# Optimization experiments

Measured on AMD Instinct MI355X. Metric: run time of the kernel, lower is better.

Reference implementation:

```python
import jax, jax.numpy as jnp
import numpy as np

INPUT_DIM = 512
HIDDEN_DIM = 1024
OUTPUT_DIM = 1000
BATCH = 256
SEQ_LEN = 256


def setup_inputs() -> dict:
    key = jax.random.key(0)
    ks = jax.random.split(key, 7)
    std = 1.0 / np.sqrt(HIDDEN_DIM)
    u = lambda k, shape: jax.random.uniform(k, shape, jnp.float32, -std, std)
    return {
        "x": jax.random.normal(ks[0], (BATCH, SEQ_LEN, INPUT_DIM), jnp.float32),
        "w_x2h": u(ks[1], (4 * HIDDEN_DIM, INPUT_DIM)),
        "b_x2h": u(ks[2], (4 * HIDDEN_DIM,)),
        "w_h2h": u(ks[3], (4 * HIDDEN_DIM, HIDDEN_DIM)),
        "b_h2h": u(ks[4], (4 * HIDDEN_DIM,)),
        "w_fc": u(ks[5], (OUTPUT_DIM, HIDDEN_DIM)),
        "b_fc": u(ks[6], (OUTPUT_DIM,)),
    }


def _lstm_last_hidden(x, w_x2h, b_x2h, w_h2h, b_h2h):
    B, T, D = x.shape
    H = w_h2h.shape[1]
    # Precompute input-to-hidden for all timesteps in one big GEMM: [B,T,4H]
    xg = jnp.einsum("btd,gd->btg", x, w_x2h) + b_x2h + b_h2h
    xg = jnp.swapaxes(xg, 0, 1)  # [T,B,4H] for scan

    def step(carry, xg_t):
        h, c = carry
        gates = xg_t + h @ w_h2h.T  # [B,4H]
        i, f, g, o = jnp.split(gates, 4, axis=1)
        i = jax.nn.sigmoid(i)
        f = jax.nn.sigmoid(f)
        g = jnp.tanh(g)
        o = jax.nn.sigmoid(o)
        c = c * f + i * g
        h = o * jnp.tanh(c)
        return (h, c), None

    h0 = jnp.zeros((B, H), x.dtype)
    c0 = jnp.zeros((B, H), x.dtype)
    (h_last, _), _ = jax.lax.scan(step, (h0, c0), xg)
    return h_last


def reference(x, w_x2h, b_x2h, w_h2h, b_h2h, w_fc, b_fc):
    h_last = _lstm_last_hidden(x, w_x2h, b_x2h, w_h2h, b_h2h)  # [B,H]
    return h_last @ w_fc.T + b_fc  # [B,OUTPUT_DIM]
```

## Files before the change

### kernel.cpp

```cpp
#include <hip/hip_runtime.h>

typedef __attribute__((ext_vector_type(8))) short short8;
typedef __attribute__((ext_vector_type(4))) float floatx4;

#define DIN  512
#define HSZ  1024
#define G4   4096
#define KTOT 1536
#define BQ   256
#define TT   256

#define MFMA __builtin_amdgcn_mfma_f32_16x16x32_bf16

__device__ __forceinline__ unsigned short f2bf(float f){
  unsigned int u = __float_as_uint(f);
  u += 0x7fffu + ((u >> 16) & 1u);
  return (unsigned short)(u >> 16);
}
__device__ __forceinline__ unsigned int pack2(float a, float b){
  return (unsigned int)f2bf(a) | ((unsigned int)f2bf(b) << 16);
}

__global__ void prep_wcat(const float* __restrict__ wx, const float* __restrict__ wh,
                          const float* __restrict__ bx, const float* __restrict__ bh,
                          unsigned short* __restrict__ Wcat, float* __restrict__ bias){
  int gid = blockIdx.x * blockDim.x + threadIdx.x;
  int idx = gid * 8;
  int g = idx / KTOT;
  int k = idx - g * KTOT;
  const float* src = (k < DIN) ? (wx + (size_t)g * DIN + k)
                               : (wh + (size_t)g * HSZ + (k - DIN));
  float4 f0 = *(const float4*)(src);
  float4 f1 = *(const float4*)(src + 4);
  uint4 v = make_uint4(pack2(f0.x,f0.y), pack2(f0.z,f0.w), pack2(f1.x,f1.y), pack2(f1.z,f1.w));
  *(uint4*)(Wcat + (size_t)g * KTOT + k) = v;
  if (gid < G4) bias[gid] = bx[gid] + bh[gid];
}

__global__ void prep_wfc(const float* __restrict__ wfc, unsigned short* __restrict__ Wfcb){
  int gid = blockIdx.x * blockDim.x + threadIdx.x;
  int idx = gid * 8;
  int n = idx >> 10;
  int k = idx & 1023;
  uint4 v;
  if (n < 1000){
    const float* src = wfc + (size_t)n * 1024 + k;
    float4 f0 = *(const float4*)(src);
    float4 f1 = *(const float4*)(src + 4);
    v = make_uint4(pack2(f0.x,f0.y), pack2(f0.z,f0.w), pack2(f1.x,f1.y), pack2(f1.z,f1.w));
  } else {
    v = make_uint4(0u, 0u, 0u, 0u);
  }
  *(uint4*)(Wfcb + idx) = v;
}

__global__ void prep_x(const float* __restrict__ x, unsigned short* __restrict__ xbf){
  int gid = blockIdx.x * 256 + threadIdx.x;
  int d8 = gid & 63;
  int b  = (gid >> 6) & 255;
  int t  = gid >> 14;
  const float* src = x + (((size_t)b * TT) + t) * DIN + d8 * 8;
  float4 f0 = *(const float4*)(src);
  float4 f1 = *(const float4*)(src + 4);
  uint4 v = make_uint4(pack2(f0.x,f0.y), pack2(f0.z,f0.w), pack2(f1.x,f1.y), pack2(f1.z,f1.w));
  *(uint4*)(xbf + (((size_t)t * BQ) + b) * DIN + d8 * 8) = v;
}

__global__ void init_misc(unsigned int* __restrict__ h0w, unsigned int* __restrict__ cnt, int ncnt){
  int gid = blockIdx.x * 256 + threadIdx.x;
  if (gid < 131072) h0w[gid] = 0u;
  if (gid < ncnt)   cnt[gid] = 0u;
}

__global__ __launch_bounds__(512, 2)
void lstm_persist(const unsigned short* __restrict__ xbf,
                  const unsigned short* __restrict__ Wcat,
                  const float* __restrict__ bias,
                  unsigned short* __restrict__ hseq,
                  unsigned int* __restrict__ cnt){
  extern __shared__ char smem[];
  char*  Ws  = smem;
  float* Gt2 = (float*)(smem + 98304);
  float* Bls = (float*)(smem + 98304 + 34816);

  const int tid  = threadIdx.x;
  const int bx   = blockIdx.x;
  const int bg   = bx >> 7;
  const int b0   = bg << 7;
  const int hb   = bx & 127;
  const int u0   = hb << 3;
  const int lane = tid & 63;
  const int w    = tid >> 6;
  const int kg   = w & 1;
  const int rg   = w >> 1;

  {
    int c  = tid >> 4;
    int ch = tid & 15;
    int grow = (c >> 3) * HSZ + u0 + (c & 7);
    const char* src = (const char*)(Wcat + (size_t)grow * KTOT);
    char* dst = Ws + c * 3072;
    int xr = (c & 7) << 4;
    #pragma unroll
    for (int q = 0; q < 12; ++q){
      int k2 = ch * 192 + q * 16;
      *(uint4*)(dst + (k2 ^ xr)) = *(const uint4*)(src + k2);
    }
    if (tid < 32) Bls[tid] = bias[(size_t)(tid >> 3) * HSZ + u0 + (tid & 7)];
  }
  __syncthreads();

  const int kq8  = (lane >> 4) * 8;
  const int cA   = lane & 15;
  const int cB   = 16 + (lane & 15);
  const char* bpA = Ws + cA * 3072; const int xorA = (cA & 7) << 4;
  const char* bpB = Ws + cB * 3072; const int xorB = (cB & 7) << 4;

  const size_t rowA0 = (size_t)(b0 + rg * 32 + (lane & 15));

  const int erow = tid >> 2;
  const int eup  = (tid & 3) * 2;
  float cst0 = 0.f, cst1 = 0.f;

  for (int t = 0; t < TT; ++t){
    const unsigned short* hin  = hseq + (size_t)t * (BQ * HSZ);
    unsigned short*       hout = hseq + (size_t)(t + 1) * (BQ * HSZ);

    floatx4 acc[2][2][2];
    #pragma unroll
    for (int ab = 0; ab < 2; ++ab)
      #pragma unroll
      for (int rf = 0; rf < 2; ++rf)
        #pragma unroll
        for (int cf = 0; cf < 2; ++cf)
          acc[ab][rf][cf] = (floatx4){0.f,0.f,0.f,0.f};

    short8 X0[8], X1[8];
    {
      const unsigned short* xr0p = xbf + ((size_t)t * BQ + rowA0) * DIN + kg * 256 + kq8;
      const unsigned short* xr1p = xr0p + 16 * DIN;
      #pragma unroll
      for (int p = 0; p < 8; ++p){
        X0[p] = *(const short8*)(xr0p + p * 32);
        X1[p] = *(const short8*)(xr1p + p * 32);
      }
    }
    __builtin_amdgcn_sched_barrier(0);

    if (t > 0){
      if (tid < 64){
        const unsigned int* cp = &cnt[(((size_t)t * 2 + bg) * 8) * 16];
        const int g16 = (lane & 7) * 16;
        while (true){
          unsigned int v = __hip_atomic_load(cp + g16, __ATOMIC_RELAXED, __HIP_MEMORY_SCOPE_AGENT);
          if (__ballot(v >= 16u) == ~0ull) break;
          __builtin_amdgcn_s_sleep(2);
        }
      }
      __syncthreads();
      asm volatile("" ::: "memory");
    }

    {
      const int bbase = kg * 512 + kq8 * 2;
      short8 bA[2], bB[2];
      bA[0] = *(const short8*)(bpA + ((bbase     ) ^ xorA));
      bB[0] = *(const short8*)(bpB + ((bbase     ) ^ xorB));
      bA[1] = *(const short8*)(bpA + ((bbase + 64) ^ xorA));
      bB[1] = *(const short8*)(bpB + ((bbase + 64) ^ xorB));
      #pragma unroll
      for (int j = 0; j < 8; ++j){
        const int sl = j & 1;
        short8 b0 = bA[sl], b1 = bB[sl];
        if (j < 6){
          int bb = bbase + (j + 2) * 64;
          bA[sl] = *(const short8*)(bpA + (bb ^ xorA));
          bB[sl] = *(const short8*)(bpB + (bb ^ xorB));
        }
        acc[sl][0][0] = MFMA(X0[j], b0, acc[sl][0][0], 0, 0, 0);
        acc[sl][0][1] = MFMA(X0[j], b1, acc[sl][0][1], 0, 0, 0);
        acc[sl][1][0] = MFMA(X1[j], b0, acc[sl][1][0], 0, 0, 0);
        acc[sl][1][1] = MFMA(X1[j], b1, acc[sl][1][1], 0, 0, 0);
      }
    }

    {
      const unsigned short* hr0 = hin + rowA0 * HSZ + kg * 512 + kq8;
      const unsigned short* hr1 = hr0 + (size_t)16 * HSZ;
      short8 A0[16], A1[16];
      #pragma unroll
      for (int p = 0; p < 16; ++p){
        A0[p] = *(const short8*)(hr0 + p * 32);
        A1[p] = *(const short8*)(hr1 + p * 32);
      }
      __builtin_amdgcn_sched_barrier(0);
      const int bbase = 1024 + kg * 1024 + kq8 * 2;
      short8 bA[2], bB[2];
      bA[0] = *(const short8*)(bpA + ((bbase     ) ^ xorA));
      bB[0] = *(const short8*)(bpB + ((bbase     ) ^ xorB));
      bA[1] = *(const short8*)(bpA + ((bbase + 64) ^ xorA));
      bB[1] = *(const short8*)(bpB + ((bbase + 64) ^ xorB));
      #pragma unroll
      for (int j = 0; j < 16; ++j){
        const int sl = j & 1;
        short8 b0 = bA[sl], b1 = bB[sl];
        if (j < 14){
          int bb = bbase + (j + 2) * 64;
          bA[sl] = *(const short8*)(bpA + (bb ^ xorA));
          bB[sl] = *(const short8*)(bpB + (bb ^ xorB));
        }
        acc[sl][0][0] = MFMA(A0[j], b0, acc[sl][0][0], 0, 0, 0);
        acc[sl][0][1] = MFMA(A0[j], b1, acc[sl][0][1], 0, 0, 0);
        acc[sl][1][0] = MFMA(A1[j], b0, acc[sl][1][0], 0, 0, 0);
        acc[sl][1][1] = MFMA(A1[j], b1, acc[sl][1][1], 0, 0, 0);
      }
    }

    {
      float* gdst = Gt2 + kg * (128 * 34);
      int r0 = rg * 32 + (lane >> 4) * 4;
      #pragma unroll
      for (int rf = 0; rf < 2; ++rf){
        floatx4 g0 = acc[0][rf][0] + acc[1][rf][0];
        floatx4 g1 = acc[0][rf][1] + acc[1][rf][1];
        #pragma unroll
        for (int r = 0; r < 4; ++r){
          gdst[(r0 + rf * 16 + r) * 34 + cA] = g0[r];
          gdst[(r0 + rf * 16 + r) * 34 + cB] = g1[r];
        }
      }
    }
    __syncthreads();

    {
      const float* g0p = Gt2 + erow * 34;
      const float* g1p = g0p + 128 * 34;
      float gi0 = g0p[     eup] + g1p[     eup] + Bls[     eup];
      float gf0 = g0p[ 8 + eup] + g1p[ 8 + eup] + Bls[ 8 + eup];
      float gg0 = g0p[16 + eup] + g1p[16 + eup] + Bls[16 + eup];
      float go0 = g0p[24 + eup] + g1p[24 + eup] + Bls[24 + eup];
      float gi1 = g0p[     eup + 1] + g1p[     eup + 1] + Bls[     eup + 1];
      float gf1 = g0p[ 8 + eup + 1] + g1p[ 8 + eup + 1] + Bls[ 8 + eup + 1];
      float gg1 = g0p[16 + eup + 1] + g1p[16 + eup + 1] + Bls[16 + eup + 1];
      float go1 = g0p[24 + eup + 1] + g1p[24 + eup + 1] + Bls[24 + eup + 1];

      float iv0 = 1.f / (1.f + __expf(-gi0));
      float fv0 = 1.f / (1.f + __expf(-gf0));
      float e20 = __expf(-2.f * fmaxf(fminf(gg0, 30.f), -30.f));
      float gv0 = (1.f - e20) / (1.f + e20);
      float ov0 = 1.f / (1.f + __expf(-go0));
      float cn0 = cst0 * fv0 + iv0 * gv0;
      cst0 = cn0;
      float ec0 = __expf(-2.f * fmaxf(fminf(cn0, 30.f), -30.f));
      float hv0 = ov0 * (1.f - ec0) / (1.f + ec0);

      float iv1 = 1.f / (1.f + __expf(-gi1));
      float fv1 = 1.f / (1.f + __expf(-gf1));
      float e21 = __expf(-2.f * fmaxf(fminf(gg1, 30.f), -30.f));
      float gv1 = (1.f - e21) / (1.f + e21);
      float ov1 = 1.f / (1.f + __expf(-go1));
      float cn1 = cst1 * fv1 + iv1 * gv1;
      cst1 = cn1;
      float ec1 = __expf(-2.f * fmaxf(fminf(cn1, 30.f), -30.f));
      float hv1 = ov1 * (1.f - ec1) / (1.f + ec1);

      __hip_atomic_store((unsigned int*)(hout + (size_t)(b0 + erow) * HSZ + u0 + eup),
                         pack2(hv0, hv1), __ATOMIC_RELAXED, __HIP_MEMORY_SCOPE_AGENT);
    }
    __syncthreads();

    if (tid == 0){
      __hip_atomic_fetch_add(&cnt[(((size_t)(t + 1) * 2 + bg) * 8 + (hb >> 4)) * 16], 1u,
                             __ATOMIC_RELAXED, __HIP_MEMORY_SCOPE_AGENT);
    }
  }
}

__global__ __launch_bounds__(256, 1)
void fc_kernel(const unsigned short* __restrict__ h, const unsigned short* __restrict__ wfc,
               const float* __restrict__ bfc, float* __restrict__ out){
  int bx = blockIdx.x, tid = threadIdx.x;
  int wave = tid >> 6, lane = tid & 63;
  int row0 = (bx >> 4) * 64 + wave * 16;
  int col0 = (bx & 15) * 64;
  int lr = lane & 15, lk = (lane >> 4) * 8;
  floatx4 acc[4] = {{0.f,0.f,0.f,0.f},{0.f,0.f,0.f,0.f},{0.f,0.f,0.f,0.f},{0.f,0.f,0.f,0.f}};
  #pragma unroll 4
  for (int ks = 0; ks < 32; ++ks){
    int k = ks * 32 + lk;
    short8 a = *(const short8*)(h + (size_t)(row0 + lr) * 1024 + k);
    #pragma unroll
    for (int fj = 0; fj < 4; ++fj){
      short8 b = *(const short8*)(wfc + (size_t)(col0 + fj * 16 + lr) * 1024 + k);
      acc[fj] = MFMA(a, b, acc[fj], 0, 0, 0);
    }
  }
  #pragma unroll
  for (int fj = 0; fj < 4; ++fj){
    int col = col0 + fj * 16 + lr;
    if (col < 1000){
      #pragma unroll
      for (int r = 0; r < 4; ++r){
        int row = row0 + (lane >> 4) * 4 + r;
        out[(size_t)row * 1000 + col] = acc[fj][r] + bfc[col];
      }
    }
  }
}

extern "C" void kernel_launch(void* const* d_in, const int* in_sizes, int n_in,
                              void* d_out, int out_size, void* d_ws, size_t ws_size,
                              hipStream_t stream){
  const float* x    = (const float*)d_in[0];
  const float* wx2h = (const float*)d_in[1];
  const float* bx2h = (const float*)d_in[2];
  const float* wh2h = (const float*)d_in[3];
  const float* bh2h = (const float*)d_in[4];
  const float* wfc  = (const float*)d_in[5];
  const float* bfc  = (const float*)d_in[6];
  float* out = (float*)d_out;
  char* ws = (char*)d_ws;

  unsigned short* Wcat = (unsigned short*)(ws + 0);
  unsigned short* Wfcb = (unsigned short*)(ws + 12582912);
  float*          bias = (float*)         (ws + 14680064);
  unsigned short* xbf  = (unsigned short*)(ws + 14696448);
  unsigned short* hseq = (unsigned short*)(ws + 81805312);
  unsigned int*   cntb = (unsigned int*)  (ws + 216547328);

  (void)hipFuncSetAttribute((const void*)lstm_persist,
                            hipFuncAttributeMaxDynamicSharedMemorySize, 133376);

  hipLaunchKernelGGL(prep_wcat, dim3(3072), dim3(256), 0, stream, wx2h, wh2h, bx2h, bh2h, Wcat, bias);
  hipLaunchKernelGGL(prep_wfc,  dim3(512),  dim3(256), 0, stream, wfc, Wfcb);
  hipLaunchKernelGGL(prep_x,    dim3(16384),dim3(256), 0, stream, x, xbf);
  hipLaunchKernelGGL(init_misc, dim3(512),  dim3(256), 0, stream,
                     (unsigned int*)hseq, cntb, (int)(263168 / 4));

  hipLaunchKernelGGL(lstm_persist, dim3(256), dim3(512), 133376, stream,
                     xbf, Wcat, bias, hseq, cntb);

  hipLaunchKernelGGL(fc_kernel, dim3(64), dim3(256), 0, stream,
                     hseq + (size_t)256 * BQ * HSZ, Wfcb, bfc, out);
}
```

Before: 3.112 ms.

## Replace whole-step barrier with per-chunk flag waits overlapping h loads and MFMA

Removes the block-wide spin on all eight producer counters followed by __syncthreads before the recurrent GEMM. Each wave now waits only on the counter for the specific 128-column chunk of h it needs, loads that chunk into a double buffer, and runs MFMAs on the previous chunk while waiting for the next. The aim is to begin recurrent work as soon as partial h is published, shortening the critical path per timestep. In exchange every lane issues its own atomic polls, there is more polling traffic, and B fragments are no longer software-prefetched.

```diff
diff --git a/kernel.cpp b/kernel.cpp
--- a/kernel.cpp
+++ b/kernel.cpp
@@ -147,20 +147,6 @@
     }
     __builtin_amdgcn_sched_barrier(0);
 
-    if (t > 0){
-      if (tid < 64){
-        const unsigned int* cp = &cnt[(((size_t)t * 2 + bg) * 8) * 16];
-        const int g16 = (lane & 7) * 16;
-        while (true){
-          unsigned int v = __hip_atomic_load(cp + g16, __ATOMIC_RELAXED, __HIP_MEMORY_SCOPE_AGENT);
-          if (__ballot(v >= 16u) == ~0ull) break;
-          __builtin_amdgcn_s_sleep(2);
-        }
-      }
-      __syncthreads();
-      asm volatile("" ::: "memory");
-    }
-
     {
       const int bbase = kg * 512 + kq8 * 2;
       short8 bA[2], bB[2];
@@ -185,35 +171,59 @@
     }
 
     {
-      const unsigned short* hr0 = hin + rowA0 * HSZ + kg * 512 + kq8;
+      const unsigned int* cbase = &cnt[(((size_t)t * 2 + bg) * 8) * 16];
+      const unsigned short* hr0 = hin + rowA0 * HSZ + kq8;
       const unsigned short* hr1 = hr0 + (size_t)16 * HSZ;
-      short8 A0[16], A1[16];
-      #pragma unroll
-      for (int p = 0; p < 16; ++p){
-        A0[p] = *(const short8*)(hr0 + p * 32);
-        A1[p] = *(const short8*)(hr1 + p * 32);
-      }
-      __builtin_amdgcn_sched_barrier(0);
-      const int bbase = 1024 + kg * 1024 + kq8 * 2;
-      short8 bA[2], bB[2];
-      bA[0] = *(const short8*)(bpA + ((bbase     ) ^ xorA));
-      bB[0] = *(const short8*)(bpB + ((bbase     ) ^ xorB));
-      bA[1] = *(const short8*)(bpA + ((bbase + 64) ^ xorA));
-      bB[1] = *(const short8*)(bpB + ((bbase + 64) ^ xorB));
-      #pragma unroll
-      for (int j = 0; j < 16; ++j){
-        const int sl = j & 1;
-        short8 b0 = bA[sl], b1 = bB[sl];
-        if (j < 14){
-          int bb = bbase + (j + 2) * 64;
-          bA[sl] = *(const short8*)(bpA + (bb ^ xorA));
-          bB[sl] = *(const short8*)(bpB + (bb ^ xorB));
-        }
-        acc[sl][0][0] = MFMA(A0[j], b0, acc[sl][0][0], 0, 0, 0);
-        acc[sl][0][1] = MFMA(A0[j], b1, acc[sl][0][1], 0, 0, 0);
-        acc[sl][1][0] = MFMA(A1[j], b0, acc[sl][1][0], 0, 0, 0);
-        acc[sl][1][1] = MFMA(A1[j], b1, acc[sl][1][1], 0, 0, 0);
-      }
+      short8 HA0[2][4], HA1[2][4];
+
+      #define WAITG(g)                                                              \
+        if (t > 0){                                                                 \
+          const unsigned int* _p = cbase + (g) * 16;                                \
+          while (__hip_atomic_load(_p, __ATOMIC_RELAXED, __HIP_MEMORY_SCOPE_AGENT)  \
+                 < 16u)                                                             \
+            __builtin_amdgcn_s_sleep(1);                                            \
+          asm volatile("" ::: "memory");                                            \
+        }
+      #define LOADCHUNK(c, buf)                                                     \
+        {                                                                           \
+          const int _ub = kg * 512 + (c) * 128;                                     \
+          _Pragma("unroll")                                                         \
+          for (int p = 0; p < 4; ++p){                                              \
+            HA0[buf][p] = *(const short8*)(hr0 + _ub + p * 32);                     \
+            HA1[buf][p] = *(const short8*)(hr1 + _ub + p * 32);                     \
+          }                                                                         \
+        }
+
+      WAITG(4 * kg);
+      LOADCHUNK(0, 0);
+      #pragma unroll
+      for (int c = 0; c < 4; ++c){
+        if (c < 3){
+          WAITG(4 * kg + c + 1);
+          if ((c + 1) & 1) { LOADCHUNK(c + 1, 1); } else { LOADCHUNK(c + 1, 0); }
+        }
+        __builtin_amdgcn_sched_barrier(0);
+        const int bbase = 1024 + kg * 1024 + c * 256 + kq8 * 2;
+        #pragma unroll
+        for (int j = 0; j < 4; ++j){
+          short8 b0 = *(const short8*)(bpA + ((bbase + j * 64) ^ xorA));
+          short8 b1 = *(const short8*)(bpB + ((bbase + j * 64) ^ xorB));
+          const int sl = j & 1;
+          if (c & 1){
+            acc[sl][0][0] = MFMA(HA0[1][j], b0, acc[sl][0][0], 0, 0, 0);
+            acc[sl][0][1] = MFMA(HA0[1][j], b1, acc[sl][0][1], 0, 0, 0);
+            acc[sl][1][0] = MFMA(HA1[1][j], b0, acc[sl][1][0], 0, 0, 0);
+            acc[sl][1][1] = MFMA(HA1[1][j], b1, acc[sl][1][1], 0, 0, 0);
+          } else {
+            acc[sl][0][0] = MFMA(HA0[0][j], b0, acc[sl][0][0], 0, 0, 0);
+            acc[sl][0][1] = MFMA(HA0[0][j], b1, acc[sl][0][1], 0, 0, 0);
+            acc[sl][1][0] = MFMA(HA1[0][j], b0, acc[sl][1][0], 0, 0, 0);
+            acc[sl][1][1] = MFMA(HA1[0][j], b1, acc[sl][1][1], 0, 0, 0);
+          }
+        }
+      }
+      #undef WAITG
+      #undef LOADCHUNK
     }
 
     {
```

Result: no change. 3.138 ms (+0.9%).
